# Kernel tuning notes

Measured on AMD Instinct MI355X. Metric: run time of the kernel, lower is better.

The kernel has to match this reference:

```python
import jax, jax.numpy as jnp
import numpy as np

B, T, C, H = 2, 2048, 1024, 16
HS = C // H  # head size = 64


def _rope_cos_sin(t, hs):
    # theta_i = 1/10000^(2(i-1)/hs) for i in [1, hs/2]
    pos = jnp.arange(t, dtype=jnp.float32)[:, None]          # [T,1]
    i = jnp.arange(1, hs // 2 + 1, dtype=jnp.float32)[None]  # [1,hs/2]
    theta = 1.0 / 10000.0 ** (2.0 * (i - 1.0) / hs)
    ang = pos * theta                                        # [T,hs/2]
    return jnp.cos(ang), jnp.sin(ang)


def _apply_rope(u, cos, sin):
    # u: [B,H,T,HS]; complex multiply on consecutive pairs
    u2 = u.reshape(*u.shape[:-1], HS // 2, 2)
    x0, x1 = u2[..., 0], u2[..., 1]
    c = cos[None, None]  # [1,1,T,hs/2]
    s = sin[None, None]
    r0 = x0 * c - x1 * s
    r1 = x0 * s + x1 * c
    return jnp.stack([r0, r1], axis=-1).reshape(u.shape)


def setup_inputs() -> dict:
    key = jax.random.key(0)
    ks = jax.random.split(key, 5)
    return {
        "x": jax.random.normal(ks[0], (B, T, C), dtype=jnp.float32),
        "W_qkv": jax.random.normal(ks[1], (C, 3 * C), dtype=jnp.float32) * 0.02,
        "b_qkv": jax.random.normal(ks[2], (3 * C,), dtype=jnp.float32) * 0.02,
        "W_proj": jax.random.normal(ks[3], (C, C), dtype=jnp.float32) * 0.02,
        "b_proj": jax.random.normal(ks[4], (C,), dtype=jnp.float32) * 0.02,
    }


def reference(x, W_qkv, b_qkv, W_proj, b_proj):
    b, t, c = x.shape
    qkv = x @ W_qkv + b_qkv                                   # [B,T,3C]
    qkv = qkv.reshape(b, t, H, 3 * HS).transpose(0, 2, 1, 3)  # [B,H,T,3*HS]
    q, k, v = jnp.split(qkv, 3, axis=-1)                      # each [B,H,T,HS]

    cos, sin = _rope_cos_sin(t, HS)
    q = _apply_rope(q, cos, sin)
    k = _apply_rope(k, cos, sin)

    att = jnp.einsum("bhqd,bhkd->bhqk", q, k) / jnp.sqrt(jnp.float32(HS))
    causal = jnp.tril(jnp.ones((t, t), dtype=bool))[None, None]
    att = jnp.where(causal, att, jnp.float32(-1e9))
    att = jax.nn.softmax(att, axis=-1)
    y = jnp.einsum("bhqk,bhkd->bhqd", att, v)                 # [B,H,T,HS]
    y = y.transpose(0, 2, 1, 3).reshape(b, t, c)
    return y @ W_proj + b_proj
```

## Files before the change

### kernel.cpp

```cpp
#include <hip/hip_runtime.h>

typedef unsigned short u16;
typedef unsigned int u32;
typedef __bf16 bf16x8 __attribute__((ext_vector_type(8)));
typedef float f32x4 __attribute__((ext_vector_type(4)));
typedef u16 u16x4 __attribute__((ext_vector_type(4)));
typedef u16 u16x8 __attribute__((ext_vector_type(8)));

__device__ __forceinline__ u16 f2bf(float f) {
  u32 u = __builtin_bit_cast(u32, f);
  u += 0x7fffu + ((u >> 16) & 1u);
  return (u16)(u >> 16);
}

__device__ __forceinline__ u32 pk2(float a, float b) {
  u32 ua = __builtin_bit_cast(u32, a) + 0x8000u;
  u32 ub = __builtin_bit_cast(u32, b) + 0x8000u;
  return __builtin_amdgcn_perm(ub, ua, 0x07060302);
}

__device__ __forceinline__ void gld16(const void* g, void* l) {
  __builtin_amdgcn_global_load_lds(
      (const __attribute__((address_space(1))) void*)g,
      (__attribute__((address_space(3))) void*)l, 16, 0, 0);
}

__global__ __launch_bounds__(256) void k_prep(
    const float* __restrict__ x, u16* __restrict__ xb,
    const float* __restrict__ Wqkv, u16* __restrict__ Wqkvt,
    const float* __restrict__ Wproj, u16* __restrict__ Wpt,
    float2* __restrict__ rope) {
  __shared__ float tile[32][33];
  const int tid = threadIdx.x;
  int bx = blockIdx.x;
  if (bx < 4096) {
    int i = (bx * 256 + tid) * 4;
    float4 v = *(const float4*)(x + i);
    u16x4 o = { f2bf(v.x), f2bf(v.y), f2bf(v.z), f2bf(v.w) };
    *(u16x4*)(xb + i) = o;
    return;
  }
  bx -= 4096;
  const float* src; u16* dst; int R, Cc, bxx, byy;
  if (bx < 3072) {
    src = Wqkv; dst = Wqkvt; R = 1024; Cc = 3072; bxx = bx % 96; byy = bx / 96;
  } else if (bx < 4096) {
    int b = bx - 3072;
    src = Wproj; dst = Wpt; R = 1024; Cc = 1024; bxx = b % 32; byy = b / 32;
  } else {
    int i = (bx - 4096) * 256 + tid;
    int t = i >> 5, d = i & 31;
    float theta = expf(-(float)d * 0.28782313662425575f);
    float ang = (float)t * theta;
    rope[i] = make_float2(cosf(ang), sinf(ang));
    return;
  }
  int xx = tid & 31, yy = tid >> 5;
  int c0 = bxx * 32, r0 = byy * 32;
  for (int i = 0; i < 4; ++i)
    tile[yy + 8 * i][xx] = src[(size_t)(r0 + yy + 8 * i) * Cc + c0 + xx];
  __syncthreads();
  for (int i = 0; i < 4; ++i)
    dst[(size_t)(c0 + yy + 8 * i) * R + r0 + xx] = f2bf(tile[xx][yy + 8 * i]);
}

__global__ __launch_bounds__(256, 4) void k_qkv(
    const u16* __restrict__ Xb,
    const u16* __restrict__ Wt,
    const float* __restrict__ bias,
    const float2* __restrict__ rope,
    u16* __restrict__ Qg,
    u16* __restrict__ Kg,
    u16* __restrict__ Vt) {
  __shared__ alignas(16) u16 smem[18432];
  u16* As = smem;
  u16* Bs = smem + 8192;
  const int tid = threadIdx.x;
  const int lane = tid & 63, w = tid >> 6;
  const int quad = lane >> 4, l15 = lane & 15;
  const int m0 = blockIdx.y * 128, n0 = blockIdx.x * 128;
  const int wm = (w & 1) * 64, wn = (w >> 1) * 64;
  const int srow = lane >> 3, sj = lane & 7;
  const int sw = (sj ^ srow) * 8;
  const f32x4 vzero = {0.f, 0.f, 0.f, 0.f};

  f32x4 acc[4][4];
  for (int i = 0; i < 4; ++i)
    for (int j = 0; j < 4; ++j) acc[i][j] = vzero;

  for (int kt = 0; kt < 1024; kt += 64) {
    __syncthreads();
    for (int i = 0; i < 4; ++i) {
      int row = w * 32 + i * 8;
      gld16(Xb + (size_t)(m0 + row + srow) * 1024 + kt + sw, &As[row * 64]);
      gld16(Wt + (size_t)(n0 + row + srow) * 1024 + kt + sw, &Bs[row * 64]);
    }
    __syncthreads();
    for (int ks = 0; ks < 2; ++ks) {
      const int cc = ((ks * 4 + quad) ^ (l15 & 7)) * 8;
      bf16x8 a[4], b[4];
      for (int mt = 0; mt < 4; ++mt)
        a[mt] = *(const bf16x8*)&As[(wm + mt * 16 + l15) * 64 + cc];
      for (int nt = 0; nt < 4; ++nt)
        b[nt] = *(const bf16x8*)&Bs[(wn + nt * 16 + l15) * 64 + cc];
      for (int nt = 0; nt < 4; ++nt)
        for (int mt = 0; mt < 4; ++mt)
          acc[nt][mt] = __builtin_amdgcn_mfma_f32_16x16x32_bf16(
              b[nt], a[mt], acc[nt][mt], 0, 0, 0);
    }
  }
  __syncthreads();

  const int half = w >> 1;
  const int nh = n0 + half * 64;
  const int region = (nh % 192) >> 6;
  u16* Eh = smem + half * 9216;
  if (region < 2) {
    const float qsc = (region == 0) ? 0.18033688011112042f : 1.0f;
    for (int nt = 0; nt < 4; ++nt) {
      float4 bv4 = *(const float4*)&bias[nh + nt * 16 + quad * 4];
      for (int mt = 0; mt < 4; ++mt) {
        int m_l = wm + mt * 16 + l15;
        int t = (m0 + m_l) & 2047;
        float4 cs = *(const float4*)&rope[t * 32 + nt * 8 + quad * 2];
        float v0 = acc[nt][mt][0] + bv4.x;
        float v1 = acc[nt][mt][1] + bv4.y;
        float v2 = acc[nt][mt][2] + bv4.z;
        float v3 = acc[nt][mt][3] + bv4.w;
        float r0 = fmaf(-v1, cs.y, v0 * cs.x) * qsc;
        float r1 = fmaf( v0, cs.y, v1 * cs.x) * qsc;
        float r2 = fmaf(-v3, cs.w, v2 * cs.z) * qsc;
        float r3 = fmaf( v2, cs.w, v3 * cs.z) * qsc;
        uint2 pv; pv.x = pk2(r0, r1); pv.y = pk2(r2, r3);
        *(uint2*)&Eh[m_l * 72 + nt * 16 + quad * 4] = pv;
      }
    }
  } else {
    for (int nt = 0; nt < 4; ++nt) {
      float4 bv4 = *(const float4*)&bias[nh + nt * 16 + quad * 4];
      for (int mt = 0; mt < 4; ++mt) {
        int m_l = wm + mt * 16 + l15;
        int cb = nt * 16 + quad * 4;
        Eh[(cb + 0) * 136 + m_l] = f2bf(acc[nt][mt][0] + bv4.x);
        Eh[(cb + 1) * 136 + m_l] = f2bf(acc[nt][mt][1] + bv4.y);
        Eh[(cb + 2) * 136 + m_l] = f2bf(acc[nt][mt][2] + bv4.z);
        Eh[(cb + 3) * 136 + m_l] = f2bf(acc[nt][mt][3] + bv4.w);
      }
    }
  }
  __syncthreads();

  const int bb = m0 >> 11, t0 = m0 & 2047;
  for (int hf = 0; hf < 2; ++hf) {
    const int nhf = n0 + hf * 64;
    const int hh = nhf / 192;
    const int reg = (nhf % 192) >> 6;
    const u16* Ef = smem + hf * 9216;
    if (reg < 2) {
      u16* dst = (reg == 0 ? Qg : Kg) +
                 ((size_t)(bb * 16 + hh) * 2048 + t0) * 64;
      int chunk = tid & 7, row0 = tid >> 3;
      for (int p = 0; p < 4; ++p) {
        int row = row0 + p * 32;
        u16x8 val = *(const u16x8*)&Ef[row * 72 + chunk * 8];
        *(u16x8*)(dst + (size_t)row * 64 + chunk * 8) = val;
      }
    } else {
      u16* dstv = Vt + (size_t)(bb * 16 + hh) * 64 * 2048 + t0;
      int mch = tid & 15, c0r = tid >> 4;
      for (int p = 0; p < 4; ++p) {
        int c = c0r + p * 16;
        u16x8 val = *(const u16x8*)&Ef[c * 136 + mch * 8];
        *(u16x8*)(dstv + (size_t)c * 2048 + mch * 8) = val;
      }
    }
  }
}

__global__ __launch_bounds__(256, 4) void k_attn(
    const u16* __restrict__ Qg, const u16* __restrict__ Kg,
    const u16* __restrict__ Vt, u16* __restrict__ Og) {
  __shared__ alignas(16) u16 Ks[2][64 * 64];
  __shared__ alignas(16) u16 Vs[2][64 * 64];
  __shared__ alignas(16) u16 Ps[64 * 64];
  const int tid = threadIdx.x, lane = tid & 63, w = tid >> 6;
  const int quad = lane >> 4, l15 = lane & 15;
  const int id = blockIdx.x;
  const int xr = id & 7, j = id >> 3;
  const int bh = (j >> 5) * 8 + xr;
  const int x32 = (j + 7 * (j >> 5)) & 31;
  const int qt = (x32 & 1) ? (x32 >> 1) : (31 - (x32 >> 1));
  const u16* Qh = Qg + (size_t)bh * 2048 * 64;
  const u16* Kh = Kg + (size_t)bh * 2048 * 64;
  const u16* Vh = Vt + (size_t)bh * 64 * 2048;
  const f32x4 vzero = {0.f, 0.f, 0.f, 0.f};
  const int myrow = w * 16;
  const int bb = bh >> 4, h = bh & 15;

  const int r8 = lane >> 3, j8 = lane & 7;
  const int sw_c = (j8 ^ r8) * 8;
  const int psw = (l15 & 7) << 1;

  for (int i = 0; i < 2; ++i) {
    int row = w * 16 + i * 8;
    gld16(Kh + (size_t)(row + r8) * 64 + sw_c, &Ks[0][row * 64]);
    gld16(Vh + (size_t)(row + r8) * 2048 + sw_c, &Vs[0][row * 64]);
  }

  const int q0 = qt * 64;
  bf16x8 aq[2];
  {
    const u16* qp = Qh + (size_t)(q0 + myrow + l15) * 64 + quad * 8;
    aq[0] = *(const bf16x8*)(qp);
    aq[1] = *(const bf16x8*)(qp + 32);
  }
  float lsum = 0.f;
  f32x4 O[4];
  for (int nt = 0; nt < 4; ++nt) O[nt] = vzero;

  int buf = 0;
  const int nk = qt + 1;
  for (int kb = 0; kb < nk; ++kb) {
    const int k0 = kb * 64;
    __syncthreads();
    if (kb + 1 < nk) {
      const int nxt = k0 + 64;
      for (int i = 0; i < 2; ++i) {
        int row = w * 16 + i * 8;
        gld16(Kh + (size_t)(nxt + row + r8) * 64 + sw_c, &Ks[buf ^ 1][row * 64]);
        gld16(Vh + (size_t)(row + r8) * 2048 + nxt + sw_c, &Vs[buf ^ 1][row * 64]);
      }
    }

    f32x4 st[4];
    for (int nt = 0; nt < 4; ++nt) st[nt] = vzero;
    for (int ks = 0; ks < 2; ++ks) {
      bf16x8 ak[4];
      for (int nt = 0; nt < 4; ++nt)
        ak[nt] = *(const bf16x8*)&Ks[buf][(nt * 16 + l15) * 64 +
                                         ((ks * 4 + quad) ^ (l15 & 7)) * 8];
      for (int nt = 0; nt < 4; ++nt)
        st[nt] = __builtin_amdgcn_mfma_f32_16x16x32_bf16(ak[nt], aq[ks], st[nt], 0, 0, 0);
    }

    const int prow = myrow + l15;
    if (kb < qt) {
      for (int nt = 0; nt < 4; ++nt) {
        float p0 = __builtin_amdgcn_exp2f(st[nt][0]);
        float p1 = __builtin_amdgcn_exp2f(st[nt][1]);
        float p2 = __builtin_amdgcn_exp2f(st[nt][2]);
        float p3 = __builtin_amdgcn_exp2f(st[nt][3]);
        lsum += (p0 + p1) + (p2 + p3);
        uint2 pv; pv.x = pk2(p0, p1); pv.y = pk2(p2, p3);
        *(uint2*)&Ps[prow * 64 + ((nt * 4 + quad) ^ psw) * 4] = pv;
      }
    } else {
      const int tq = q0 + myrow + l15;
      const int kbase = k0 + quad * 4;
      for (int nt = 0; nt < 4; ++nt) {
        float p[4];
        for (int r = 0; r < 4; ++r) {
          float pv = __builtin_amdgcn_exp2f(st[nt][r]);
          p[r] = (kbase + nt * 16 + r <= tq) ? pv : 0.f;
          lsum += p[r];
        }
        uint2 pv; pv.x = pk2(p[0], p[1]); pv.y = pk2(p[2], p[3]);
        *(uint2*)&Ps[prow * 64 + ((nt * 4 + quad) ^ psw) * 4] = pv;
      }
    }

    for (int ks = 0; ks < 2; ++ks) {
      bf16x8 a = *(const bf16x8*)&Ps[prow * 64 + ((ks * 8 + quad * 2) ^ psw) * 4];
      bf16x8 bv[4];
      for (int nt = 0; nt < 4; ++nt)
        bv[nt] = *(const bf16x8*)&Vs[buf][(nt * 16 + l15) * 64 +
                                         ((ks * 4 + quad) ^ (l15 & 7)) * 8];
      for (int nt = 0; nt < 4; ++nt)
        O[nt] = __builtin_amdgcn_mfma_f32_16x16x32_bf16(a, bv[nt], O[nt], 0, 0, 0);
    }
    buf ^= 1;
  }

  float ls = lsum;
  ls += __shfl_xor(ls, 16, 64);
  ls += __shfl_xor(ls, 32, 64);
  float inv[4];
  for (int r = 0; r < 4; ++r)
    inv[r] = 1.0f / __shfl(ls, quad * 4 + r, 16);

  for (int nt = 0; nt < 4; ++nt)
    for (int r = 0; r < 4; ++r) {
      int row = myrow + quad * 4 + r;
      int col = nt * 16 + l15;
      int up = (col >> 2) ^ ((row & 7) << 1);
      Ps[row * 64 + up * 4 + (col & 3)] = f2bf(O[nt][r] * inv[r]);
    }
  __syncthreads();
  u16* dst = Og + ((size_t)bb * 2048 + q0) * 1024 + h * 64;
  int chunk = tid & 7, row0 = tid >> 3;
  for (int p = 0; p < 2; ++p) {
    int row = row0 + p * 32;
    int up = (chunk * 2) ^ ((row & 7) << 1);
    u16x8 val = *(const u16x8*)&Ps[row * 64 + up * 4];
    *(u16x8*)(dst + (size_t)row * 1024 + chunk * 8) = val;
  }
}

__global__ __launch_bounds__(256, 4) void k_proj(
    const u16* __restrict__ Ag,
    const u16* __restrict__ Wt,
    const float* __restrict__ bias,
    float* __restrict__ out) {
  __shared__ alignas(16) u16 As[64 * 64];
  __shared__ alignas(16) u16 Bs[128 * 64];
  const int tid = threadIdx.x;
  const int lane = tid & 63, w = tid >> 6;
  const int quad = lane >> 4, l15 = lane & 15;
  const int m0 = blockIdx.y * 64, n0 = blockIdx.x * 128;
  const int wm = (w & 1) * 32, wn = (w >> 1) * 64;
  const int srow = lane >> 3, sj = lane & 7;
  const int sw = (sj ^ srow) * 8;
  const f32x4 vzero = {0.f, 0.f, 0.f, 0.f};

  f32x4 acc[2][4];
  for (int i = 0; i < 2; ++i)
    for (int j = 0; j < 4; ++j) acc[i][j] = vzero;

  for (int kt = 0; kt < 1024; kt += 64) {
    __syncthreads();
    for (int i = 0; i < 2; ++i) {
      int row = w * 16 + i * 8;
      gld16(Ag + (size_t)(m0 + row + srow) * 1024 + kt + sw, &As[row * 64]);
    }
    for (int i = 0; i < 4; ++i) {
      int row = w * 32 + i * 8;
      gld16(Wt + (size_t)(n0 + row + srow) * 1024 + kt + sw, &Bs[row * 64]);
    }
    __syncthreads();
    for (int ks = 0; ks < 2; ++ks) {
      const int cc = ((ks * 4 + quad) ^ (l15 & 7)) * 8;
      bf16x8 a[2], b[4];
      for (int mt = 0; mt < 2; ++mt)
        a[mt] = *(const bf16x8*)&As[(wm + mt * 16 + l15) * 64 + cc];
      for (int nt = 0; nt < 4; ++nt)
        b[nt] = *(const bf16x8*)&Bs[(wn + nt * 16 + l15) * 64 + cc];
      for (int mt = 0; mt < 2; ++mt)
        for (int nt = 0; nt < 4; ++nt)
          acc[mt][nt] = __builtin_amdgcn_mfma_f32_16x16x32_bf16(
              a[mt], b[nt], acc[mt][nt], 0, 0, 0);
    }
  }

  for (int nt = 0; nt < 4; ++nt) {
    int n = n0 + wn + nt * 16 + l15;
    float bv = bias[n];
    for (int mt = 0; mt < 2; ++mt)
      for (int r = 0; r < 4; ++r) {
        int m = m0 + wm + mt * 16 + quad * 4 + r;
        out[(size_t)m * 1024 + n] = acc[mt][nt][r] + bv;
      }
  }
}

extern "C" void kernel_launch(void* const* d_in, const int* in_sizes, int n_in,
                              void* d_out, int out_size, void* d_ws, size_t ws_size,
                              hipStream_t stream) {
  (void)in_sizes; (void)n_in; (void)out_size; (void)ws_size;
  const float* x     = (const float*)d_in[0];
  const float* Wqkv  = (const float*)d_in[1];
  const float* bqkv  = (const float*)d_in[2];
  const float* Wproj = (const float*)d_in[3];
  const float* bproj = (const float*)d_in[4];
  float* out = (float*)d_out;

  char* ws = (char*)d_ws;
  size_t off = 0;
  u16* Xb    = (u16*)(ws + off); off += (size_t)4096 * 1024 * 2;
  u16* Wqkvt = (u16*)(ws + off); off += (size_t)3072 * 1024 * 2;
  u16* Wpt   = (u16*)(ws + off); off += (size_t)1024 * 1024 * 2;
  u16* Qg    = (u16*)(ws + off); off += (size_t)2 * 16 * 2048 * 64 * 2;
  u16* Kg    = (u16*)(ws + off); off += (size_t)2 * 16 * 2048 * 64 * 2;
  u16* Vt    = (u16*)(ws + off); off += (size_t)2 * 16 * 64 * 2048 * 2;
  u16* Att   = (u16*)(ws + off); off += (size_t)4096 * 1024 * 2;
  float2* rope = (float2*)(ws + off); off += (size_t)2048 * 32 * sizeof(float2);

  k_prep<<<8448, 256, 0, stream>>>(x, Xb, Wqkv, Wqkvt, Wproj, Wpt, rope);
  k_qkv<<<dim3(24, 32), 256, 0, stream>>>(Xb, Wqkvt, bqkv, rope, Qg, Kg, Vt);
  k_attn<<<1024, 256, 0, stream>>>(Qg, Kg, Vt, Att);
  k_proj<<<dim3(8, 64), 256, 0, stream>>>(Att, Wpt, bproj, out);
}
```

Before: 175.7 us.

## Restructure attention into 128-row paired causal tiles with 32x32 MFMA and register P

The attention kernel now gives each block two complementary 128-query tiles (tA and 15-tA), so every block does the same causal work, and launches 256 blocks instead of 1024. It moves from 16x16x32 to 32x32x16 MFMA, with each wave owning 32 query rows. The P matrix is repacked in registers with v_permlane32_swap instead of a round trip through shared memory. Manual vmcnt waits and raw s_barrier calls drive a double-buffered K/V prefetch. The aims are to remove LDS traffic for P, even out causal load imbalance, and raise MFMA efficiency, at the cost of fewer blocks, lower occupancy (launch bounds 2) and more register pressure.

```diff
diff --git a/kernel.cpp b/kernel.cpp
--- a/kernel.cpp
+++ b/kernel.cpp
@@ -4,6 +4,8 @@
 typedef unsigned int u32;
 typedef __bf16 bf16x8 __attribute__((ext_vector_type(8)));
 typedef float f32x4 __attribute__((ext_vector_type(4)));
+typedef float f32x16 __attribute__((ext_vector_type(16)));
+typedef u32 u32x4 __attribute__((ext_vector_type(4)));
 typedef u16 u16x4 __attribute__((ext_vector_type(4)));
 typedef u16 u16x8 __attribute__((ext_vector_type(8)));
 
@@ -177,132 +179,160 @@
   }
 }
 
-__global__ __launch_bounds__(256, 4) void k_attn(
+__global__ __launch_bounds__(256, 2) void k_attn(
     const u16* __restrict__ Qg, const u16* __restrict__ Kg,
     const u16* __restrict__ Vt, u16* __restrict__ Og) {
   __shared__ alignas(16) u16 Ks[2][64 * 64];
   __shared__ alignas(16) u16 Vs[2][64 * 64];
-  __shared__ alignas(16) u16 Ps[64 * 64];
+  __shared__ float Ls[4][32];
   const int tid = threadIdx.x, lane = tid & 63, w = tid >> 6;
-  const int quad = lane >> 4, l15 = lane & 15;
+  const int q32 = lane & 31, hi = lane >> 5;
   const int id = blockIdx.x;
   const int xr = id & 7, j = id >> 3;
-  const int bh = (j >> 5) * 8 + xr;
-  const int x32 = (j + 7 * (j >> 5)) & 31;
-  const int qt = (x32 & 1) ? (x32 >> 1) : (31 - (x32 >> 1));
+  const int bh = (j >> 3) * 8 + xr;
+  const int tA = j & 7, tB = 15 - tA;
+  const int nkbA = 2 * tA + 2;
   const u16* Qh = Qg + (size_t)bh * 2048 * 64;
   const u16* Kh = Kg + (size_t)bh * 2048 * 64;
   const u16* Vh = Vt + (size_t)bh * 64 * 2048;
-  const f32x4 vzero = {0.f, 0.f, 0.f, 0.f};
-  const int myrow = w * 16;
   const int bb = bh >> 4, h = bh & 15;
 
   const int r8 = lane >> 3, j8 = lane & 7;
   const int sw_c = (j8 ^ r8) * 8;
-  const int psw = (l15 & 7) << 1;
-
-  for (int i = 0; i < 2; ++i) {
-    int row = w * 16 + i * 8;
-    gld16(Kh + (size_t)(row + r8) * 64 + sw_c, &Ks[0][row * 64]);
-    gld16(Vh + (size_t)(row + r8) * 2048 + sw_c, &Vs[0][row * 64]);
-  }
-
-  const int q0 = qt * 64;
-  bf16x8 aq[2];
+
+  auto stage = [&](int i, int b) {
+    const int kk0 = (i < nkbA ? i : i - nkbA) * 64;
+    for (int t = 0; t < 2; ++t) {
+      int row = w * 16 + t * 8;
+      gld16(Kh + (size_t)(kk0 + row + r8) * 64 + sw_c, &Ks[b][row * 64]);
+      gld16(Vh + (size_t)(row + r8) * 2048 + kk0 + sw_c, &Vs[b][row * 64]);
+    }
+  };
+
+  bf16x8 aq[4];
   {
-    const u16* qp = Qh + (size_t)(q0 + myrow + l15) * 64 + quad * 8;
-    aq[0] = *(const bf16x8*)(qp);
-    aq[1] = *(const bf16x8*)(qp + 32);
-  }
+    const u16* qp = Qh + (size_t)(tA * 128 + w * 32 + q32) * 64 + hi * 8;
+#pragma unroll
+    for (int ds = 0; ds < 4; ++ds) aq[ds] = *(const bf16x8*)(qp + ds * 16);
+  }
+  asm volatile("" ::: "memory");
+  stage(0, 0);
+  stage(1, 1);
+
+  f32x16 O0 = {}, O1 = {};
   float lsum = 0.f;
-  f32x4 O[4];
-  for (int nt = 0; nt < 4; ++nt) O[nt] = vzero;
-
-  int buf = 0;
-  const int nk = qt + 1;
-  for (int kb = 0; kb < nk; ++kb) {
-    const int k0 = kb * 64;
-    __syncthreads();
-    if (kb + 1 < nk) {
-      const int nxt = k0 + 64;
-      for (int i = 0; i < 2; ++i) {
-        int row = w * 16 + i * 8;
-        gld16(Kh + (size_t)(nxt + row + r8) * 64 + sw_c, &Ks[buf ^ 1][row * 64]);
-        gld16(Vh + (size_t)(row + r8) * 2048 + nxt + sw_c, &Vs[buf ^ 1][row * 64]);
-      }
-    }
-
-    f32x4 st[4];
-    for (int nt = 0; nt < 4; ++nt) st[nt] = vzero;
-    for (int ks = 0; ks < 2; ++ks) {
-      bf16x8 ak[4];
-      for (int nt = 0; nt < 4; ++nt)
-        ak[nt] = *(const bf16x8*)&Ks[buf][(nt * 16 + l15) * 64 +
-                                         ((ks * 4 + quad) ^ (l15 & 7)) * 8];
-      for (int nt = 0; nt < 4; ++nt)
-        st[nt] = __builtin_amdgcn_mfma_f32_16x16x32_bf16(ak[nt], aq[ks], st[nt], 0, 0, 0);
-    }
-
-    const int prow = myrow + l15;
-    if (kb < qt) {
-      for (int nt = 0; nt < 4; ++nt) {
-        float p0 = __builtin_amdgcn_exp2f(st[nt][0]);
-        float p1 = __builtin_amdgcn_exp2f(st[nt][1]);
-        float p2 = __builtin_amdgcn_exp2f(st[nt][2]);
-        float p3 = __builtin_amdgcn_exp2f(st[nt][3]);
-        lsum += (p0 + p1) + (p2 + p3);
-        uint2 pv; pv.x = pk2(p0, p1); pv.y = pk2(p2, p3);
-        *(uint2*)&Ps[prow * 64 + ((nt * 4 + quad) ^ psw) * 4] = pv;
-      }
-    } else {
-      const int tq = q0 + myrow + l15;
-      const int kbase = k0 + quad * 4;
-      for (int nt = 0; nt < 4; ++nt) {
-        float p[4];
-        for (int r = 0; r < 4; ++r) {
-          float pv = __builtin_amdgcn_exp2f(st[nt][r]);
-          p[r] = (kbase + nt * 16 + r <= tq) ? pv : 0.f;
-          lsum += p[r];
+  int qb = tA * 128;
+  int kcap = 2 * tA + (w >> 1);
+
+  for (int it = 0; it < 34; ++it) {
+    const int buf = it & 1;
+    if (it == 33) asm volatile("s_waitcnt vmcnt(0)" ::: "memory");
+    else          asm volatile("s_waitcnt vmcnt(4)" ::: "memory");
+    asm volatile("s_barrier" ::: "memory");
+
+    const bool isA = it < nkbA;
+    const int kb = isA ? it : it - nkbA;
+
+    if (kb <= kcap) {
+      const int k0 = kb * 64;
+      f32x16 st0 = {}, st1 = {};
+#pragma unroll
+      for (int ds = 0; ds < 4; ++ds) {
+        const int c = ((ds * 2 + hi) ^ (q32 & 7)) * 8;
+        bf16x8 ak0 = *(const bf16x8*)&Ks[buf][q32 * 64 + c];
+        bf16x8 ak1 = *(const bf16x8*)&Ks[buf][(32 + q32) * 64 + c];
+        st0 = __builtin_amdgcn_mfma_f32_32x32x16_bf16(ak0, aq[ds], st0, 0, 0, 0);
+        st1 = __builtin_amdgcn_mfma_f32_32x32x16_bf16(ak1, aq[ds], st1, 0, 0, 0);
+      }
+
+      float p0[16], p1[16];
+      if (kb == kcap) {
+        const int q = qb + w * 32 + q32;
+#pragma unroll
+        for (int r = 0; r < 16; ++r) {
+          int kk = k0 + (r & 3) + 8 * (r >> 2) + 4 * hi;
+          float e0 = __builtin_amdgcn_exp2f(st0[r]);
+          float e1 = __builtin_amdgcn_exp2f(st1[r]);
+          p0[r] = (kk <= q) ? e0 : 0.f;
+          p1[r] = (kk + 32 <= q) ? e1 : 0.f;
+          lsum += p0[r] + p1[r];
         }
-        uint2 pv; pv.x = pk2(p[0], p[1]); pv.y = pk2(p[2], p[3]);
-        *(uint2*)&Ps[prow * 64 + ((nt * 4 + quad) ^ psw) * 4] = pv;
-      }
-    }
-
-    for (int ks = 0; ks < 2; ++ks) {
-      bf16x8 a = *(const bf16x8*)&Ps[prow * 64 + ((ks * 8 + quad * 2) ^ psw) * 4];
-      bf16x8 bv[4];
-      for (int nt = 0; nt < 4; ++nt)
-        bv[nt] = *(const bf16x8*)&Vs[buf][(nt * 16 + l15) * 64 +
-                                         ((ks * 4 + quad) ^ (l15 & 7)) * 8];
-      for (int nt = 0; nt < 4; ++nt)
-        O[nt] = __builtin_amdgcn_mfma_f32_16x16x32_bf16(a, bv[nt], O[nt], 0, 0, 0);
-    }
-    buf ^= 1;
-  }
-
-  float ls = lsum;
-  ls += __shfl_xor(ls, 16, 64);
-  ls += __shfl_xor(ls, 32, 64);
-  float inv[4];
-  for (int r = 0; r < 4; ++r)
-    inv[r] = 1.0f / __shfl(ls, quad * 4 + r, 16);
-
-  for (int nt = 0; nt < 4; ++nt)
-    for (int r = 0; r < 4; ++r) {
-      int row = myrow + quad * 4 + r;
-      int col = nt * 16 + l15;
-      int up = (col >> 2) ^ ((row & 7) << 1);
-      Ps[row * 64 + up * 4 + (col & 3)] = f2bf(O[nt][r] * inv[r]);
-    }
-  __syncthreads();
-  u16* dst = Og + ((size_t)bb * 2048 + q0) * 1024 + h * 64;
-  int chunk = tid & 7, row0 = tid >> 3;
-  for (int p = 0; p < 2; ++p) {
-    int row = row0 + p * 32;
-    int up = (chunk * 2) ^ ((row & 7) << 1);
-    u16x8 val = *(const u16x8*)&Ps[row * 64 + up * 4];
-    *(u16x8*)(dst + (size_t)row * 1024 + chunk * 8) = val;
+      } else {
+#pragma unroll
+        for (int r = 0; r < 16; ++r) {
+          p0[r] = __builtin_amdgcn_exp2f(st0[r]);
+          p1[r] = __builtin_amdgcn_exp2f(st1[r]);
+          lsum += p0[r] + p1[r];
+        }
+      }
+
+      u32 paw[4][4];
+#pragma unroll
+      for (int kt = 0; kt < 2; ++kt) {
+        const float* P = kt ? p1 : p0;
+#pragma unroll
+        for (int kl = 0; kl < 2; ++kl) {
+          const int b0i = kl * 8;
+          u32 a0 = pk2(P[b0i + 0], P[b0i + 1]);
+          u32 b0 = pk2(P[b0i + 4], P[b0i + 5]);
+          u32 a1 = pk2(P[b0i + 2], P[b0i + 3]);
+          u32 b1 = pk2(P[b0i + 6], P[b0i + 7]);
+          asm volatile("v_permlane32_swap_b32 %0, %1" : "+v"(a0), "+v"(b0));
+          asm volatile("v_permlane32_swap_b32 %0, %1" : "+v"(a1), "+v"(b1));
+          const int s = kt * 2 + kl;
+          paw[s][0] = a0; paw[s][1] = a1; paw[s][2] = b0; paw[s][3] = b1;
+        }
+      }
+
+#pragma unroll
+      for (int s = 0; s < 4; ++s) {
+        u32x4 pw = { paw[s][0], paw[s][1], paw[s][2], paw[s][3] };
+        bf16x8 pa = __builtin_bit_cast(bf16x8, pw);
+        const int c = ((s * 2 + hi) ^ (q32 & 7)) * 8;
+        bf16x8 bv0 = *(const bf16x8*)&Vs[buf][q32 * 64 + c];
+        bf16x8 bv1 = *(const bf16x8*)&Vs[buf][(32 + q32) * 64 + c];
+        O0 = __builtin_amdgcn_mfma_f32_32x32x16_bf16(pa, bv0, O0, 0, 0, 0);
+        O1 = __builtin_amdgcn_mfma_f32_32x32x16_bf16(pa, bv1, O1, 0, 0, 0);
+      }
+    }
+
+    asm volatile("s_barrier" ::: "memory");
+    if (it + 2 < 34) stage(it + 2, buf);
+
+    if (it == nkbA - 1) {
+      float lt = lsum + __shfl_xor(lsum, 32, 64);
+      float invl = 1.0f / lt;
+      if (lane < 32) Ls[w][q32] = invl;
+      u16* dst = Og + ((size_t)bb * 2048 + tA * 128 + w * 32) * 1024 + h * 64 + q32;
+#pragma unroll
+      for (int r = 0; r < 16; ++r) {
+        int qp = (r & 3) + 8 * (r >> 2) + 4 * hi;
+        float iv = Ls[w][qp];
+        dst[(size_t)qp * 1024]      = f2bf(O0[r] * iv);
+        dst[(size_t)qp * 1024 + 32] = f2bf(O1[r] * iv);
+      }
+      lsum = 0.f;
+      O0 = {}; O1 = {};
+      const u16* qp = Qh + (size_t)(tB * 128 + w * 32 + q32) * 64 + hi * 8;
+#pragma unroll
+      for (int ds = 0; ds < 4; ++ds) aq[ds] = *(const bf16x8*)(qp + ds * 16);
+      qb = tB * 128;
+      kcap = 2 * tB + (w >> 1);
+    }
+  }
+
+  {
+    float lt = lsum + __shfl_xor(lsum, 32, 64);
+    float invl = 1.0f / lt;
+    if (lane < 32) Ls[w][q32] = invl;
+    u16* dst = Og + ((size_t)bb * 2048 + tB * 128 + w * 32) * 1024 + h * 64 + q32;
+#pragma unroll
+    for (int r = 0; r < 16; ++r) {
+      int qp = (r & 3) + 8 * (r >> 2) + 4 * hi;
+      float iv = Ls[w][qp];
+      dst[(size_t)qp * 1024]      = f2bf(O0[r] * iv);
+      dst[(size_t)qp * 1024 + 32] = f2bf(O1[r] * iv);
+    }
   }
 }
 
@@ -386,6 +416,6 @@
 
   k_prep<<<8448, 256, 0, stream>>>(x, Xb, Wqkv, Wqkvt, Wproj, Wpt, rope);
   k_qkv<<<dim3(24, 32), 256, 0, stream>>>(Xb, Wqkvt, bqkv, rope, Qg, Kg, Vt);
-  k_attn<<<1024, 256, 0, stream>>>(Qg, Kg, Vt, Att);
+  k_attn<<<256, 256, 0, stream>>>(Qg, Kg, Vt, Att);
   k_proj<<<dim3(8, 64), 256, 0, stream>>>(Att, Wpt, bproj, out);
 }
```

After: 171.3 us. 1.03x faster.
